# Kernel tuning notes

Measured on AMD Instinct MI355X. Metric: run time of the kernel, lower is better.

Reference implementation:

```python
import jax, jax.numpy as jnp
import numpy as np

B, S, D = 16, 2048, 256
SCALE = 1.0 / np.sqrt(D).astype(np.float32)

def setup_inputs() -> dict:
    key = jax.random.key(0)
    k1, k2, k3, k4 = jax.random.split(key, 4)
    x = jax.random.normal(k1, (B, S, D), dtype=jnp.float32)
    w_qkv = jax.random.normal(k2, (3 * D, D), dtype=jnp.float32) * (1.0 / np.sqrt(D))
    w_out = jax.random.normal(k3, (D, D), dtype=jnp.float32) * (1.0 / np.sqrt(D))
    b_out = jax.random.normal(k4, (D,), dtype=jnp.float32) * 0.01
    return {"x": x, "w_qkv": w_qkv, "w_out": w_out, "b_out": b_out}

def reference(x, w_qkv, w_out, b_out):
    # qkv: [B, S, 3D] = x @ W_qkv^T (torch Linear convention)
    qkv = jnp.einsum('bsd,ed->bse', x, w_qkv)
    q, k, v = jnp.split(qkv, 3, axis=-1)  # each [B, S, D]
    scores = jnp.einsum('bsd,btd->bst', q, k) * SCALE  # [B, S, S]
    attn = jax.nn.softmax(scores, axis=-1)  # dropout = identity (eval mode)
    ctx = jnp.einsum('bst,btd->bsd', attn, v)  # [B, S, D]
    out = jnp.einsum('bsd,ed->bse', ctx, w_out) + b_out
    return out
```

## Files before the change

kernel.cpp:

```cpp
#include <hip/hip_runtime.h>
#include <hip/hip_bf16.h>


typedef short bf16x8 __attribute__((ext_vector_type(8)));
typedef float f32x4 __attribute__((ext_vector_type(4)));

#define MFMA16(a, b, c) __builtin_amdgcn_mfma_f32_16x16x32_bf16((a), (b), (c), 0, 0, 0)

__device__ __forceinline__ unsigned short f2bf(float f) {
  unsigned int x;
  __builtin_memcpy(&x, &f, 4);
  x = x + 0x7fffu + ((x >> 16) & 1u);
  return (unsigned short)(x >> 16);
}
__device__ __forceinline__ unsigned int pack2(float a, float b) {
  float2 t;
  t.x = a;
  t.y = b;
  __hip_bfloat162 h = __float22bfloat162_rn(t);
  unsigned int u;
  __builtin_memcpy(&u, &h, 4);
  return u;
}

typedef __attribute__((address_space(3))) void as3_void;
typedef __attribute__((address_space(1))) const void as1_void;
__device__ __forceinline__ void gl_lds16(const void* g, void* l) {
  __builtin_amdgcn_global_load_lds((as1_void*)(unsigned long long)g,
                                   (as3_void*)(unsigned int)(unsigned long long)l,
                                   16, 0, 0);
}

__global__ __launch_bounds__(256, 1) void qkv_kernel(
    const float* __restrict__ X, const float* __restrict__ W,
    unsigned short* __restrict__ Q, unsigned short* __restrict__ Kp,
    unsigned short* __restrict__ Vt) {
  __shared__ unsigned short Al[128 * 256];
  __shared__ unsigned short Bl[128 * 256];
  const int m0 = blockIdx.x * 128;
  const int t = threadIdx.x;
  const int w = t >> 6, lane = t & 63, lo = lane & 15, quad = lane >> 4;
  const int aw = (w >> 1) * 64, bw = (w & 1) * 64;

#pragma unroll
  for (int r = 0; r < 16; ++r) {
    int ci = r * 256 + t;
    int row = ci >> 5, c = ci & 31;
    int s = (c & 24) | ((c ^ (row & 7)) & 7);
    const float* xp = X + (size_t)(m0 + row) * 256 + c * 8;
    float4 a0 = *(const float4*)xp, a1 = *(const float4*)(xp + 4);
    uint4 ua;
    ua.x = pack2(a0.x, a0.y);
    ua.y = pack2(a0.z, a0.w);
    ua.z = pack2(a1.x, a1.y);
    ua.w = pack2(a1.z, a1.w);
    *(uint4*)(&Al[row * 256 + s * 8]) = ua;
  }

  for (int n = 0; n < 6; ++n) {
    const int n0 = n * 128;
    if (n > 0) __syncthreads();
#pragma unroll
    for (int r = 0; r < 16; ++r) {
      int ci = r * 256 + t;
      int row = ci >> 5, c = ci & 31;
      int s = (c & 24) | ((c ^ (row & 7)) & 7);
      const float* wp = W + (size_t)(n0 + row) * 256 + c * 8;
      float4 b0 = *(const float4*)wp, b1 = *(const float4*)(wp + 4);
      uint4 ub;
      ub.x = pack2(b0.x, b0.y);
      ub.y = pack2(b0.z, b0.w);
      ub.z = pack2(b1.x, b1.y);
      ub.w = pack2(b1.z, b1.w);
      *(uint4*)(&Bl[row * 256 + s * 8]) = ub;
    }
    __syncthreads();

    f32x4 zero4 = {0.f, 0.f, 0.f, 0.f};
    f32x4 acc[4][4];
#pragma unroll
    for (int i = 0; i < 4; i++)
#pragma unroll
      for (int j = 0; j < 4; j++) acc[i][j] = zero4;

#pragma unroll
    for (int kc = 0; kc < 8; ++kc) {
      const int c = kc * 4 + quad;
      const int jj = (c & 24) | ((c ^ (lo & 7)) & 7);
      bf16x8 af[4], bfr[4];
#pragma unroll
      for (int mt = 0; mt < 4; ++mt)
        af[mt] = *(const bf16x8*)(&Al[(aw + mt * 16 + lo) * 256 + jj * 8]);
#pragma unroll
      for (int nt = 0; nt < 4; ++nt)
        bfr[nt] = *(const bf16x8*)(&Bl[(bw + nt * 16 + lo) * 256 + jj * 8]);
#pragma unroll
      for (int mt = 0; mt < 4; ++mt)
#pragma unroll
        for (int nt = 0; nt < 4; ++nt)
          acc[mt][nt] = MFMA16(af[mt], bfr[nt], acc[mt][nt]);
    }

    const int mb = m0 + aw, nb = n0 + bw;
    if (n0 < 256) {
#pragma unroll
      for (int mt = 0; mt < 4; ++mt)
#pragma unroll
        for (int nt = 0; nt < 4; ++nt) {
          int m = mb + mt * 16 + quad * 4;
          int nn = nb + nt * 16 + lo;
          unsigned short* p = Q + (size_t)m * 256 + nn;
          p[0] = f2bf(acc[mt][nt][0]);
          p[256] = f2bf(acc[mt][nt][1]);
          p[512] = f2bf(acc[mt][nt][2]);
          p[768] = f2bf(acc[mt][nt][3]);
        }
    } else if (n0 < 512) {
#pragma unroll
      for (int mt = 0; mt < 4; ++mt)
#pragma unroll
        for (int nt = 0; nt < 4; ++nt) {
          int m = mb + mt * 16 + quad * 4;
          int nn = nb + nt * 16 + lo - 256;
          unsigned short* p = Kp + (size_t)m * 256 + nn;
          p[0] = f2bf(acc[mt][nt][0]);
          p[256] = f2bf(acc[mt][nt][1]);
          p[512] = f2bf(acc[mt][nt][2]);
          p[768] = f2bf(acc[mt][nt][3]);
        }
    } else {
#pragma unroll
      for (int mt = 0; mt < 4; ++mt)
#pragma unroll
        for (int nt = 0; nt < 4; ++nt) {
          int m = mb + mt * 16 + quad * 4;
          int d = nb + nt * 16 + lo - 512;
          int b = m >> 11, s = m & 2047;
          uint2 v;
          v.x = pack2(acc[mt][nt][0], acc[mt][nt][1]);
          v.y = pack2(acc[mt][nt][2], acc[mt][nt][3]);
          *(uint2*)(Vt + ((size_t)(b * 256 + d)) * 2048 + s) = v;
        }
    }
  }
}

__global__ __launch_bounds__(512, 2) void attn_kernel(
    const unsigned short* __restrict__ Q, const unsigned short* __restrict__ K,
    const unsigned short* __restrict__ Vt, unsigned short* __restrict__ C) {
  __shared__ __attribute__((aligned(16))) unsigned short smem[65536];
  const int id = blockIdx.x;
  const int b = id & 15;
  const int qt = id >> 4;
  const int t = threadIdx.x;
  const int w = t >> 6, lane = t & 63, lo = lane & 15, quad = lane >> 4;
  constexpr float SCALE_LOG2E = 0.0625f * 1.4426950408889634f;

  const unsigned short* Kb = K + (size_t)b * 2048 * 256;
  const unsigned short* Vb = Vt + (size_t)b * 256 * 2048;

  unsigned int gkoff[4], gvoff[4];
  int loK[4], loV[4];
#pragma unroll
  for (int r = 0; r < 4; ++r) {
    int ck = r * 512 + t;
    int row = ck >> 5, j = ck & 31;
    int srcj = (j & 16) | ((j ^ (row & 15)) & 15);
    gkoff[r] = (unsigned int)((row * 256 + srcj * 8) * 2);
    loK[r] = __builtin_amdgcn_readfirstlane((r * 512 + w * 64) * 8);

    int cv = r * 512 + t;
    int d = cv >> 3, slot = cv & 7;
    int g = slot ^ (d & 7);
    gvoff[r] = (unsigned int)((d * 2048 + g * 8) * 2);
    loV[r] = __builtin_amdgcn_readfirstlane(16384 + (r * 512 + w * 64) * 8);
  }

  const int qrow = b * 2048 + qt * 128 + w * 16 + lo;
  const unsigned short* qp = Q + (size_t)qrow * 256;
  bf16x8 qf[8];
#pragma unroll
  for (int ks = 0; ks < 8; ++ks)
    qf[ks] = *(const bf16x8*)(qp + ks * 32 + quad * 8);

  f32x4 zero4 = {0.f, 0.f, 0.f, 0.f};
  f32x4 oacc[16];
#pragma unroll
  for (int i = 0; i < 16; i++) oacc[i] = zero4;
  float m_run = -1e30f, l_run = 0.f;

#pragma unroll
  for (int r = 0; r < 4; ++r) {
    gl_lds16((const char*)Kb + gkoff[r], &smem[loK[r]]);
    gkoff[r] += 64 * 256 * 2;
  }
#pragma unroll
  for (int r = 0; r < 4; ++r) {
    gl_lds16((const char*)Vb + gvoff[r], &smem[loV[r]]);
    gvoff[r] += 64 * 2;
  }

  for (int it = 0; it < 32; ++it) {
    asm volatile("s_waitcnt vmcnt(0)" ::: "memory");
    __syncthreads();
    if (it < 31) {
      const int pn = ((it + 1) & 1) * 32768;
#pragma unroll
      for (int r = 0; r < 4; ++r) {
        gl_lds16((const char*)Kb + gkoff[r], &smem[pn + loK[r]]);
        gkoff[r] += 64 * 256 * 2;
      }
#pragma unroll
      for (int r = 0; r < 4; ++r) {
        gl_lds16((const char*)Vb + gvoff[r], &smem[pn + loV[r]]);
        gvoff[r] += 64 * 2;
      }
    }
    const unsigned short* Kl = smem + (it & 1) * 32768;
    const unsigned short* Vl = Kl + 16384;

    f32x4 sacc[4];
#pragma unroll
    for (int r = 0; r < 4; ++r) sacc[r] = zero4;
    __builtin_amdgcn_s_setprio(1);
#pragma unroll
    for (int ks = 0; ks < 8; ++ks) {
      const int c = ks * 4 + quad;
      const int jj = (c & 16) | ((c ^ lo) & 15);
#pragma unroll
      for (int r = 0; r < 4; ++r) {
        bf16x8 kf = *(const bf16x8*)(&Kl[(r * 16 + lo) * 256 + jj * 8]);
        sacc[r] = MFMA16(kf, qf[ks], sacc[r]);
      }
    }
    __builtin_amdgcn_s_setprio(0);

    float p[4][4];
    float cmax = -1e30f;
#pragma unroll
    for (int r = 0; r < 4; r++)
#pragma unroll
      for (int i = 0; i < 4; i++) {
        p[r][i] = sacc[r][i] * SCALE_LOG2E;
        cmax = fmaxf(cmax, p[r][i]);
      }
    cmax = fmaxf(cmax, __shfl_xor(cmax, 16));
    cmax = fmaxf(cmax, __shfl_xor(cmax, 32));
    if (!__all(cmax <= m_run + 8.f)) {
      float mnew = fmaxf(m_run, cmax);
      float alpha = exp2f(m_run - mnew);
      l_run *= alpha;
#pragma unroll
      for (int i = 0; i < 16; i++) oacc[i] *= alpha;
      m_run = mnew;
    }
    float rsum = 0.f;
#pragma unroll
    for (int r = 0; r < 4; r++)
#pragma unroll
      for (int i = 0; i < 4; i++) {
        p[r][i] = exp2f(p[r][i] - m_run);
        rsum += p[r][i];
      }
    rsum += __shfl_xor(rsum, 16);
    rsum += __shfl_xor(rsum, 32);
    l_run += rsum;

    unsigned int pk[4][2];
#pragma unroll
    for (int r = 0; r < 4; r++) {
      pk[r][0] = pack2(p[r][0], p[r][1]);
      pk[r][1] = pack2(p[r][2], p[r][3]);
    }

#pragma unroll
    for (int ks2 = 0; ks2 < 2; ++ks2) {
      union {
        unsigned int u[4];
        bf16x8 v;
      } cvt;
#pragma unroll
      for (int dd = 0; dd < 4; ++dd) {
        int src = lo + 16 * ((2 * quad + (dd >> 1)) & 3);
        unsigned int v0 = (unsigned int)__shfl((int)pk[2 * ks2][dd & 1], src);
        unsigned int v1 = (unsigned int)__shfl((int)pk[2 * ks2 + 1][dd & 1], src);
        cvt.u[dd] = (quad >> 1) ? v1 : v0;
      }
      bf16x8 pf = cvt.v;
      __builtin_amdgcn_s_setprio(1);
#pragma unroll
      for (int dt = 0; dt < 16; ++dt) {
        int slot = (ks2 * 4 + quad) ^ (lo & 7);
        bf16x8 vf = *(const bf16x8*)(&Vl[(dt * 16 + lo) * 64 + slot * 8]);
        oacc[dt] = MFMA16(vf, pf, oacc[dt]);
      }
      __builtin_amdgcn_s_setprio(0);
    }
  }

  float inv = 1.0f / l_run;
  unsigned short* cp = C + (size_t)qrow * 256;
#pragma unroll
  for (int dt = 0; dt < 16; ++dt) {
    uint2 v;
    v.x = pack2(oacc[dt][0] * inv, oacc[dt][1] * inv);
    v.y = pack2(oacc[dt][2] * inv, oacc[dt][3] * inv);
    *(uint2*)(cp + dt * 16 + quad * 4) = v;
  }
}

__global__ __launch_bounds__(256, 3) void proj_kernel(
    const unsigned short* __restrict__ Xc, const float* __restrict__ W,
    const float* __restrict__ bias, float* __restrict__ out) {
  __shared__ unsigned short Al[128 * 64];
  __shared__ unsigned short Bl[128 * 64];
  const int n0 = blockIdx.x * 128;
  const int m0 = blockIdx.y * 128;
  const int t = threadIdx.x;
  const int w = t >> 6, lane = t & 63, lo = lane & 15, quad = lane >> 4;
  const int aw = (w >> 1) * 64, bw = (w & 1) * 64;

  f32x4 zero4 = {0.f, 0.f, 0.f, 0.f};
  f32x4 acc[4][4];
#pragma unroll
  for (int i = 0; i < 4; i++)
#pragma unroll
    for (int j = 0; j < 4; j++) acc[i][j] = zero4;

  for (int kb = 0; kb < 4; ++kb) {
    const int k0 = kb * 64;
#pragma unroll
    for (int rr = 0; rr < 4; ++rr) {
      int ci = rr * 256 + t;
      int row = ci >> 3, c = ci & 7, cs = c ^ (row & 7);
      *(int4*)(&Al[row * 64 + cs * 8]) =
          *(const int4*)(Xc + (size_t)(m0 + row) * 256 + k0 + c * 8);
      const float* wp = W + (size_t)(n0 + row) * 256 + k0 + c * 8;
      float4 b0 = *(const float4*)wp, b1 = *(const float4*)(wp + 4);
      uint4 ub;
      ub.x = pack2(b0.x, b0.y);
      ub.y = pack2(b0.z, b0.w);
      ub.z = pack2(b1.x, b1.y);
      ub.w = pack2(b1.z, b1.w);
      *(uint4*)(&Bl[row * 64 + cs * 8]) = ub;
    }
    __syncthreads();
#pragma unroll
    for (int ks = 0; ks < 2; ++ks) {
      const int c = ks * 4 + quad, cs = c ^ (lo & 7);
      bf16x8 af[4], bfr[4];
#pragma unroll
      for (int mt = 0; mt < 4; ++mt)
        af[mt] = *(const bf16x8*)(&Al[(aw + mt * 16 + lo) * 64 + cs * 8]);
#pragma unroll
      for (int nt = 0; nt < 4; ++nt)
        bfr[nt] = *(const bf16x8*)(&Bl[(bw + nt * 16 + lo) * 64 + cs * 8]);
#pragma unroll
      for (int mt = 0; mt < 4; ++mt)
#pragma unroll
        for (int nt = 0; nt < 4; ++nt)
          acc[mt][nt] = MFMA16(af[mt], bfr[nt], acc[mt][nt]);
    }
    __syncthreads();
  }

  const int mb = m0 + aw, nb = n0 + bw;
#pragma unroll
  for (int mt = 0; mt < 4; ++mt)
#pragma unroll
    for (int nt = 0; nt < 4; ++nt) {
      int m = mb + mt * 16 + quad * 4;
      int n = nb + nt * 16 + lo;
      float bv = bias[n];
      float* p = out + (size_t)m * 256 + n;
      p[0] = acc[mt][nt][0] + bv;
      p[256] = acc[mt][nt][1] + bv;
      p[512] = acc[mt][nt][2] + bv;
      p[768] = acc[mt][nt][3] + bv;
    }
}

extern "C" void kernel_launch(void* const* d_in, const int* in_sizes, int n_in,
                              void* d_out, int out_size, void* d_ws, size_t ws_size,
                              hipStream_t stream) {
  const float* X = (const float*)d_in[0];
  const float* Wq = (const float*)d_in[1];
  const float* Wo = (const float*)d_in[2];
  const float* Bo = (const float*)d_in[3];
  float* out = (float*)d_out;
  unsigned short* ws = (unsigned short*)d_ws;

  const size_t NE = (size_t)16 * 2048 * 256;
  unsigned short* Qb = ws;
  unsigned short* Kb = ws + NE;
  unsigned short* Vt = ws + 2 * NE;
  unsigned short* Cx = ws;

  qkv_kernel<<<dim3(256), 256, 0, stream>>>(X, Wq, Qb, Kb, Vt);
  attn_kernel<<<dim3(256), 512, 0, stream>>>(Qb, Kb, Vt, Cx);
  proj_kernel<<<dim3(2, 256), 256, 0, stream>>>(Cx, Wo, Bo, out);
}
```

Before: 215.8 us.

## Use 512-thread blocks for QKV and restructure projection to stage full-K A tile once

The QKV GEMM moves from 4 to 8 waves per block, each wave computing a 64x32 tile instead of 64x64, which halves per-thread load and compute work. The projection kernel is rewritten to mirror the QKV kernel. Each block owns 128 rows with the full K=256 A tile loaded once into LDS through global_load_lds, then loops over both N halves, replacing the 2x256 grid of K-chunked blocks. This aims to raise wave parallelism and remove redundant A reloads, at the cost of larger LDS use and lower occupancy per CU for the projection.

```diff
diff --git a/kernel.cpp b/kernel.cpp
--- a/kernel.cpp
+++ b/kernel.cpp
@@ -31,7 +31,7 @@
                                    16, 0, 0);
 }
 
-__global__ __launch_bounds__(256, 1) void qkv_kernel(
+__global__ __launch_bounds__(512, 1) void qkv_kernel(
     const float* __restrict__ X, const float* __restrict__ W,
     unsigned short* __restrict__ Q, unsigned short* __restrict__ Kp,
     unsigned short* __restrict__ Vt) {
@@ -40,11 +40,11 @@
   const int m0 = blockIdx.x * 128;
   const int t = threadIdx.x;
   const int w = t >> 6, lane = t & 63, lo = lane & 15, quad = lane >> 4;
-  const int aw = (w >> 1) * 64, bw = (w & 1) * 64;
-
-#pragma unroll
-  for (int r = 0; r < 16; ++r) {
-    int ci = r * 256 + t;
+  const int wr = (w >> 2) * 64, wc = (w & 3) * 32;
+
+#pragma unroll
+  for (int r = 0; r < 8; ++r) {
+    int ci = r * 512 + t;
     int row = ci >> 5, c = ci & 31;
     int s = (c & 24) | ((c ^ (row & 7)) & 7);
     const float* xp = X + (size_t)(m0 + row) * 256 + c * 8;
@@ -61,8 +61,8 @@
     const int n0 = n * 128;
     if (n > 0) __syncthreads();
 #pragma unroll
-    for (int r = 0; r < 16; ++r) {
-      int ci = r * 256 + t;
+    for (int r = 0; r < 8; ++r) {
+      int ci = r * 512 + t;
       int row = ci >> 5, c = ci & 31;
       int s = (c & 24) | ((c ^ (row & 7)) & 7);
       const float* wp = W + (size_t)(n0 + row) * 256 + c * 8;
@@ -77,36 +77,36 @@
     __syncthreads();
 
     f32x4 zero4 = {0.f, 0.f, 0.f, 0.f};
-    f32x4 acc[4][4];
+    f32x4 acc[4][2];
 #pragma unroll
     for (int i = 0; i < 4; i++)
 #pragma unroll
-      for (int j = 0; j < 4; j++) acc[i][j] = zero4;
+      for (int j = 0; j < 2; j++) acc[i][j] = zero4;
 
 #pragma unroll
     for (int kc = 0; kc < 8; ++kc) {
       const int c = kc * 4 + quad;
       const int jj = (c & 24) | ((c ^ (lo & 7)) & 7);
-      bf16x8 af[4], bfr[4];
-#pragma unroll
-      for (int mt = 0; mt < 4; ++mt)
-        af[mt] = *(const bf16x8*)(&Al[(aw + mt * 16 + lo) * 256 + jj * 8]);
-#pragma unroll
-      for (int nt = 0; nt < 4; ++nt)
-        bfr[nt] = *(const bf16x8*)(&Bl[(bw + nt * 16 + lo) * 256 + jj * 8]);
-#pragma unroll
-      for (int mt = 0; mt < 4; ++mt)
-#pragma unroll
-        for (int nt = 0; nt < 4; ++nt)
+      bf16x8 af[4], bfr[2];
+#pragma unroll
+      for (int mt = 0; mt < 4; ++mt)
+        af[mt] = *(const bf16x8*)(&Al[(wr + mt * 16 + lo) * 256 + jj * 8]);
+#pragma unroll
+      for (int nt = 0; nt < 2; ++nt)
+        bfr[nt] = *(const bf16x8*)(&Bl[(wc + nt * 16 + lo) * 256 + jj * 8]);
+#pragma unroll
+      for (int mt = 0; mt < 4; ++mt)
+#pragma unroll
+        for (int nt = 0; nt < 2; ++nt)
           acc[mt][nt] = MFMA16(af[mt], bfr[nt], acc[mt][nt]);
     }
 
-    const int mb = m0 + aw, nb = n0 + bw;
+    const int mb = m0 + wr, nb = n0 + wc;
     if (n0 < 256) {
 #pragma unroll
       for (int mt = 0; mt < 4; ++mt)
 #pragma unroll
-        for (int nt = 0; nt < 4; ++nt) {
+        for (int nt = 0; nt < 2; ++nt) {
           int m = mb + mt * 16 + quad * 4;
           int nn = nb + nt * 16 + lo;
           unsigned short* p = Q + (size_t)m * 256 + nn;
@@ -119,7 +119,7 @@
 #pragma unroll
       for (int mt = 0; mt < 4; ++mt)
 #pragma unroll
-        for (int nt = 0; nt < 4; ++nt) {
+        for (int nt = 0; nt < 2; ++nt) {
           int m = mb + mt * 16 + quad * 4;
           int nn = nb + nt * 16 + lo - 256;
           unsigned short* p = Kp + (size_t)m * 256 + nn;
@@ -132,7 +132,7 @@
 #pragma unroll
       for (int mt = 0; mt < 4; ++mt)
 #pragma unroll
-        for (int nt = 0; nt < 4; ++nt) {
+        for (int nt = 0; nt < 2; ++nt) {
           int m = mb + mt * 16 + quad * 4;
           int d = nb + nt * 16 + lo - 512;
           int b = m >> 11, s = m & 2047;
@@ -309,75 +309,87 @@
   }
 }
 
-__global__ __launch_bounds__(256, 3) void proj_kernel(
+__global__ __launch_bounds__(512, 1) void proj_kernel(
     const unsigned short* __restrict__ Xc, const float* __restrict__ W,
     const float* __restrict__ bias, float* __restrict__ out) {
-  __shared__ unsigned short Al[128 * 64];
-  __shared__ unsigned short Bl[128 * 64];
-  const int n0 = blockIdx.x * 128;
-  const int m0 = blockIdx.y * 128;
+  __shared__ unsigned short Al[128 * 256];
+  __shared__ unsigned short Bl[128 * 256];
+  const int m0 = blockIdx.x * 128;
   const int t = threadIdx.x;
   const int w = t >> 6, lane = t & 63, lo = lane & 15, quad = lane >> 4;
-  const int aw = (w >> 1) * 64, bw = (w & 1) * 64;
-
-  f32x4 zero4 = {0.f, 0.f, 0.f, 0.f};
-  f32x4 acc[4][4];
-#pragma unroll
-  for (int i = 0; i < 4; i++)
-#pragma unroll
-    for (int j = 0; j < 4; j++) acc[i][j] = zero4;
-
-  for (int kb = 0; kb < 4; ++kb) {
-    const int k0 = kb * 64;
-#pragma unroll
-    for (int rr = 0; rr < 4; ++rr) {
-      int ci = rr * 256 + t;
-      int row = ci >> 3, c = ci & 7, cs = c ^ (row & 7);
-      *(int4*)(&Al[row * 64 + cs * 8]) =
-          *(const int4*)(Xc + (size_t)(m0 + row) * 256 + k0 + c * 8);
-      const float* wp = W + (size_t)(n0 + row) * 256 + k0 + c * 8;
+  const int wr = (w >> 2) * 64, wc = (w & 3) * 32;
+
+  const unsigned short* Xb = Xc + (size_t)m0 * 256;
+#pragma unroll
+  for (int r = 0; r < 8; ++r) {
+    int idx = r * 512 + t;
+    int row = idx >> 5, sc = idx & 31;
+    int c = (sc & 24) | ((sc ^ (row & 7)) & 7);
+    int lofs = __builtin_amdgcn_readfirstlane((r * 512 + w * 64) * 8);
+    gl_lds16(Xb + (size_t)row * 256 + c * 8, &Al[lofs]);
+  }
+
+  for (int n = 0; n < 2; ++n) {
+    const int n0 = n * 128;
+    if (n > 0) __syncthreads();
+#pragma unroll
+    for (int r = 0; r < 8; ++r) {
+      int ci = r * 512 + t;
+      int row = ci >> 5, c = ci & 31;
+      int s = (c & 24) | ((c ^ (row & 7)) & 7);
+      const float* wp = W + (size_t)(n0 + row) * 256 + c * 8;
       float4 b0 = *(const float4*)wp, b1 = *(const float4*)(wp + 4);
       uint4 ub;
       ub.x = pack2(b0.x, b0.y);
       ub.y = pack2(b0.z, b0.w);
       ub.z = pack2(b1.x, b1.y);
       ub.w = pack2(b1.z, b1.w);
-      *(uint4*)(&Bl[row * 64 + cs * 8]) = ub;
-    }
+      *(uint4*)(&Bl[row * 256 + s * 8]) = ub;
+    }
+    if (n == 0) asm volatile("s_waitcnt vmcnt(0)" ::: "memory");
     __syncthreads();
-#pragma unroll
-    for (int ks = 0; ks < 2; ++ks) {
-      const int c = ks * 4 + quad, cs = c ^ (lo & 7);
-      bf16x8 af[4], bfr[4];
-#pragma unroll
-      for (int mt = 0; mt < 4; ++mt)
-        af[mt] = *(const bf16x8*)(&Al[(aw + mt * 16 + lo) * 64 + cs * 8]);
-#pragma unroll
-      for (int nt = 0; nt < 4; ++nt)
-        bfr[nt] = *(const bf16x8*)(&Bl[(bw + nt * 16 + lo) * 64 + cs * 8]);
-#pragma unroll
-      for (int mt = 0; mt < 4; ++mt)
-#pragma unroll
-        for (int nt = 0; nt < 4; ++nt)
+
+    f32x4 zero4 = {0.f, 0.f, 0.f, 0.f};
+    f32x4 acc[4][2];
+#pragma unroll
+    for (int i = 0; i < 4; i++)
+#pragma unroll
+      for (int j = 0; j < 2; j++) acc[i][j] = zero4;
+
+#pragma unroll
+    for (int kc = 0; kc < 8; ++kc) {
+      const int c = kc * 4 + quad;
+      const int jj = (c & 24) | ((c ^ (lo & 7)) & 7);
+      bf16x8 af[4], bfr[2];
+#pragma unroll
+      for (int mt = 0; mt < 4; ++mt)
+        af[mt] = *(const bf16x8*)(&Al[(wr + mt * 16 + lo) * 256 + jj * 8]);
+#pragma unroll
+      for (int nt = 0; nt < 2; ++nt)
+        bfr[nt] = *(const bf16x8*)(&Bl[(wc + nt * 16 + lo) * 256 + jj * 8]);
+#pragma unroll
+      for (int mt = 0; mt < 4; ++mt)
+#pragma unroll
+        for (int nt = 0; nt < 2; ++nt)
           acc[mt][nt] = MFMA16(af[mt], bfr[nt], acc[mt][nt]);
     }
-    __syncthreads();
-  }
-
-  const int mb = m0 + aw, nb = n0 + bw;
-#pragma unroll
-  for (int mt = 0; mt < 4; ++mt)
-#pragma unroll
-    for (int nt = 0; nt < 4; ++nt) {
-      int m = mb + mt * 16 + quad * 4;
-      int n = nb + nt * 16 + lo;
-      float bv = bias[n];
-      float* p = out + (size_t)m * 256 + n;
-      p[0] = acc[mt][nt][0] + bv;
-      p[256] = acc[mt][nt][1] + bv;
-      p[512] = acc[mt][nt][2] + bv;
-      p[768] = acc[mt][nt][3] + bv;
-    }
+
+    const int mb = m0 + wr, nb = n0 + wc;
+#pragma unroll
+    for (int nt = 0; nt < 2; ++nt) {
+      int nn = nb + nt * 16 + lo;
+      float bv = bias[nn];
+#pragma unroll
+      for (int mt = 0; mt < 4; ++mt) {
+        int m = mb + mt * 16 + quad * 4;
+        float* p = out + (size_t)m * 256 + nn;
+        p[0] = acc[mt][nt][0] + bv;
+        p[256] = acc[mt][nt][1] + bv;
+        p[512] = acc[mt][nt][2] + bv;
+        p[768] = acc[mt][nt][3] + bv;
+      }
+    }
+  }
 }
 
 extern "C" void kernel_launch(void* const* d_in, const int* in_sizes, int n_in,
@@ -396,7 +408,7 @@
   unsigned short* Vt = ws + 2 * NE;
   unsigned short* Cx = ws;
 
-  qkv_kernel<<<dim3(256), 256, 0, stream>>>(X, Wq, Qb, Kb, Vt);
+  qkv_kernel<<<dim3(256), 512, 0, stream>>>(X, Wq, Qb, Kb, Vt);
   attn_kernel<<<dim3(256), 512, 0, stream>>>(Qb, Kb, Vt, Cx);
-  proj_kernel<<<dim3(2, 256), 256, 0, stream>>>(Cx, Wo, Bo, out);
-}
+  proj_kernel<<<dim3(256), 512, 0, stream>>>(Cx, Wo, Bo, out);
+}
```

After: 214.7 us. No clear change (-0.5%).
